# Kernel optimization log

Measured on AMD Instinct MI355X. Metric: run time of the kernel, lower is better.

The kernel has to match this reference:

```python
import math
import jax, jax.numpy as jnp
import numpy as np

NUM_BINS = 8
TRANS = 8
LEFT, RIGHT = -1.0, 1.0
MIN_W = MIN_H = MIN_D = 1.0e-4


def setup_inputs() -> dict:
    key = jax.random.key(0)
    ks = jax.random.split(key, 8)
    B, D, H, OUT = 524288, 16, 256, TRANS * (3 * NUM_BINS - 1)
    x = jax.random.uniform(ks[0], (B, D), jnp.float32, -0.99, 0.99)
    W0 = jax.random.normal(ks[1], (8, H), jnp.float32) * (1.0 / math.sqrt(8))
    b0 = jnp.zeros((H,), jnp.float32)
    W1 = jax.random.normal(ks[2], (H, H), jnp.float32) * (1.0 / math.sqrt(H))
    b1 = jnp.zeros((H,), jnp.float32)
    Wout = jax.random.normal(ks[3], (H, OUT), jnp.float32) * (0.1 / math.sqrt(H))
    bout = jnp.zeros((OUT,), jnp.float32)
    return {"x": x, "W0": W0, "b0": b0, "W1": W1, "b1": b1, "Wout": Wout, "bout": bout}


def _rq_spline(x, raw_w, raw_h, raw_d):
    # x: [B, T]; raw_w/raw_h: [B, T, K]; raw_d: [B, T, K-1]
    span = RIGHT - LEFT
    const = math.log(math.exp(1.0 - MIN_D) - 1.0)
    widths = jax.nn.softmax(raw_w, axis=-1)
    heights = jax.nn.softmax(raw_h, axis=-1)
    derivs = jax.nn.softplus(raw_d + const) + MIN_D
    widths = span * (MIN_W + (1.0 - MIN_W * NUM_BINS) * widths)
    heights = span * (MIN_H + (1.0 - MIN_H * NUM_BINS) * heights)
    edge_x = LEFT + jnp.pad(jnp.cumsum(widths, axis=-1), ((0, 0), (0, 0), (1, 0)))
    edge_y = LEFT + jnp.pad(jnp.cumsum(heights, axis=-1), ((0, 0), (0, 0), (1, 0)))
    derivs = jnp.pad(derivs, ((0, 0), (0, 0), (1, 1)), constant_values=1.0)
    out_mask = (x <= LEFT + 1e-3) | (x >= RIGHT - 1e-3)
    x_in = jnp.where(out_mask, 0.0, x)
    # searchsorted(right=True) - 1 == count of edges <= x_in, minus 1
    idx = jnp.clip(jnp.sum(edge_x <= x_in[..., None], axis=-1) - 1, 0, NUM_BINS - 1)
    g = lambda a: jnp.take_along_axis(a, idx[..., None], axis=-1)[..., 0]
    xk, yk = g(edge_x), g(edge_y)
    wk, hk = g(widths), g(heights)
    dk, dk1 = g(derivs), g(derivs[..., 1:])
    sk = hk / wk
    eps = (x_in - xk) / wk
    eps_term = eps * (1.0 - eps)
    eps2 = eps * eps
    beta = sk + (dk1 + dk - 2.0 * sk) * eps_term
    alpha = hk * (sk * eps2 + dk * eps_term)
    output = jnp.where(out_mask, x, yk + alpha / beta)
    logdet = (2.0 * jnp.log(sk)
              + jnp.log(dk1 * eps2 + 2.0 * sk * eps_term + dk * (1.0 - eps) ** 2)
              - 2.0 * jnp.log(beta))
    logdet = jnp.where(out_mask, 0.0, logdet)
    return output, logdet


def reference(x, W0, b0, W1, b1, Wout, bout):
    x1 = x[..., :TRANS]   # transformed half (mask == True)
    x2 = x[..., TRANS:]   # conditioning half
    h = jax.nn.relu(x2 @ W0 + b0)
    h = jax.nn.relu(h @ W1 + b1)
    raw = (h @ Wout + bout).reshape(x.shape[0], TRANS, 3 * NUM_BINS - 1)
    raw_w = raw[..., :NUM_BINS]
    raw_h = raw[..., NUM_BINS:2 * NUM_BINS]
    raw_d = raw[..., 2 * NUM_BINS:]
    y1, logdet = _rq_spline(x1, raw_w, raw_h, raw_d)
    out = jnp.concatenate([y1, x2], axis=-1)
    return out, jnp.sum(logdet, axis=-1)
```

## Files before the change

### kernel.cpp

```cpp
#include <hip/hip_runtime.h>
#include <hip/hip_bf16.h>


typedef __bf16 bf16x8 __attribute__((ext_vector_type(8)));
typedef float  f32x4  __attribute__((ext_vector_type(4)));

#define MFMA16(a,b,c) __builtin_amdgcn_mfma_f32_16x16x32_bf16((a),(b),(c),0,0,0)

#define SW_W1_OFF 8192
#define SW_WO_OFF 73728
#define SW_TOTAL  122880

#define HSTRIDE 264
#define RSTRIDE 200

__global__ void prep_kernel(const float* __restrict__ W0,
                            const float* __restrict__ W1,
                            const float* __restrict__ Wout,
                            __bf16* __restrict__ sw)
{
  int i = blockIdx.x * 256 + threadIdx.x;
  if (i >= SW_TOTAL) return;
  const float* src; int K, N, NT, li;
  if (i < SW_W1_OFF)      { src = W0;   K = 8;   N = 256; NT = 16; li = i; }
  else if (i < SW_WO_OFF) { src = W1;   K = 256; N = 256; NT = 16; li = i - SW_W1_OFF; }
  else                    { src = Wout; K = 256; N = 184; NT = 12; li = i - SW_WO_OFF; }
  int j    = li & 7;
  int l    = (li >> 3) & 63;
  int rest = li >> 9;
  int nt   = rest % NT;
  int kb   = rest / NT;
  int k = kb * 32 + ((l >> 4) << 3) + j;
  int n = nt * 16 + (l & 15);
  float v = (k < K && n < N) ? src[k * N + n] : 0.0f;
  sw[i] = (__bf16)v;
}

__global__ __launch_bounds__(512, 4)
void fused_kernel(const float* __restrict__ x,
                  const float* __restrict__ b0v,
                  const float* __restrict__ b1v,
                  const float* __restrict__ boutv,
                  const __bf16* __restrict__ sw,
                  float* __restrict__ out,
                  int nrows)
{
  __shared__ __align__(16) unsigned char smem[2 * 64 * HSTRIDE * 2];
  __bf16* h1   = (__bf16*)smem;
  __bf16* h2   = (__bf16*)(smem + 64 * HSTRIDE * 2);
  __bf16* rawb = h1;
  float*  ldet = (float*)h2;

  const int tid  = threadIdx.x;
  const int wave = tid >> 6;
  const int lane = tid & 63;
  const int quad = lane >> 4;
  const int l16  = lane & 15;
  const int row0 = blockIdx.x * 64;

  const __bf16* swW1 = sw + SW_W1_OFF;
  const __bf16* swWo = sw + SW_WO_OFF;

  const f32x4 z4 = {0.f, 0.f, 0.f, 0.f};

  {
    bf16x8 a1[4];
    #pragma unroll
    for (int mt = 0; mt < 4; mt++){
      const float* xp = x + (long)(row0 + mt*16 + l16) * 16 + 8;
      float4 u = *(const float4*)xp;
      float4 v = *(const float4*)(xp + 4);
      bf16x8 a;
      a[0]=(__bf16)u.x; a[1]=(__bf16)u.y; a[2]=(__bf16)u.z; a[3]=(__bf16)u.w;
      a[4]=(__bf16)v.x; a[5]=(__bf16)v.y; a[6]=(__bf16)v.z; a[7]=(__bf16)v.w;
      a1[mt] = a;
    }
    f32x4 acc[4][2];
    #pragma unroll
    for (int mt=0;mt<4;mt++){ acc[mt][0]=z4; acc[mt][1]=z4; }
    #pragma unroll
    for (int nt=0;nt<2;nt++){
      int ntg = wave*2 + nt;
      bf16x8 b = *(const bf16x8*)(sw + (ntg*64 + lane)*8);
      #pragma unroll
      for (int mt=0;mt<4;mt++) acc[mt][nt] = MFMA16(a1[mt], b, acc[mt][nt]);
    }
    #pragma unroll
    for (int nt=0;nt<2;nt++){
      int col = wave*32 + nt*16 + l16;
      float bias = b0v[col];
      #pragma unroll
      for (int mt=0;mt<4;mt++)
        #pragma unroll
        for (int r=0;r<4;r++){
          int row = mt*16 + quad*4 + r;
          h1[row*HSTRIDE + col] = (__bf16)fmaxf(acc[mt][nt][r] + bias, 0.f);
        }
    }
  }
  __syncthreads();

  {
    f32x4 acc[4][2];
    #pragma unroll
    for (int mt=0;mt<4;mt++){ acc[mt][0]=z4; acc[mt][1]=z4; }
    #pragma unroll
    for (int kb=0;kb<8;kb++){
      bf16x8 af[4];
      #pragma unroll
      for (int mt=0;mt<4;mt++){
        int row = mt*16 + l16;
        af[mt] = *(const bf16x8*)(h1 + row*HSTRIDE + kb*32 + quad*8);
      }
      #pragma unroll
      for (int nt=0;nt<2;nt++){
        int ntg = wave*2 + nt;
        bf16x8 b = *(const bf16x8*)(swW1 + ((kb*16 + ntg)*64 + lane)*8);
        #pragma unroll
        for (int mt=0;mt<4;mt++) acc[mt][nt] = MFMA16(af[mt], b, acc[mt][nt]);
      }
    }
    #pragma unroll
    for (int nt=0;nt<2;nt++){
      int col = wave*32 + nt*16 + l16;
      float bias = b1v[col];
      #pragma unroll
      for (int mt=0;mt<4;mt++)
        #pragma unroll
        for (int r=0;r<4;r++){
          int row = mt*16 + quad*4 + r;
          h2[row*HSTRIDE + col] = (__bf16)fmaxf(acc[mt][nt][r] + bias, 0.f);
        }
    }
  }
  __syncthreads();

  {
    f32x4 acc[4][2];
    #pragma unroll
    for (int mt=0;mt<4;mt++){ acc[mt][0]=z4; acc[mt][1]=z4; }
    const bool has2 = (wave < 4);
    #pragma unroll
    for (int kb=0;kb<8;kb++){
      bf16x8 af[4];
      #pragma unroll
      for (int mt=0;mt<4;mt++){
        int row = mt*16 + l16;
        af[mt] = *(const bf16x8*)(h2 + row*HSTRIDE + kb*32 + quad*8);
      }
      bf16x8 b0 = *(const bf16x8*)(swWo + ((kb*12 + wave)*64 + lane)*8);
      #pragma unroll
      for (int mt=0;mt<4;mt++) acc[mt][0] = MFMA16(af[mt], b0, acc[mt][0]);
      if (has2){
        bf16x8 b1 = *(const bf16x8*)(swWo + ((kb*12 + wave + 8)*64 + lane)*8);
        #pragma unroll
        for (int mt=0;mt<4;mt++) acc[mt][1] = MFMA16(af[mt], b1, acc[mt][1]);
      }
    }
    #pragma unroll
    for (int s=0;s<2;s++){
      if (s == 1 && !has2) break;
      int ntg = s ? (wave + 8) : wave;
      int col = ntg*16 + l16;
      if (col < 184){
        int t = (col * 713) >> 14;
        float bias = boutv[col];
        #pragma unroll
        for (int mt=0;mt<4;mt++)
          #pragma unroll
          for (int r=0;r<4;r++){
            int row = mt*16 + quad*4 + r;
            rawb[row*RSTRIDE + col + t] = (__bf16)(acc[mt][s][r] + bias);
          }
      }
    }
  }
  __syncthreads();

  {
    int row = tid >> 3;
    int t   = tid & 7;
    long gr = row0 + row;
    float xv = x[gr*16 + t];
    out[gr*16 + 8 + t] = x[gr*16 + 8 + t];

    const __bf16* rr = rawb + row*RSTRIDE + t*24;
    bf16x8 v0 = *(const bf16x8*)(rr);
    bf16x8 v1 = *(const bf16x8*)(rr + 8);
    bf16x8 v2 = *(const bf16x8*)(rr + 16);

    float ew[8], eh[8];
    float sw_ = 0.f, sh_ = 0.f;
    #pragma unroll
    for (int i=0;i<8;i++){ ew[i] = __expf((float)v0[i]); sw_ += ew[i]; }
    #pragma unroll
    for (int i=0;i<8;i++){ eh[i] = __expf((float)v1[i]); sh_ += eh[i]; }
    float cw = 1.9984f * __builtin_amdgcn_rcpf(sw_);
    float ch = 1.9984f * __builtin_amdgcn_rcpf(sh_);

    float d[9];
    d[0] = 1.f; d[8] = 1.f;
    #pragma unroll
    for (int i=0;i<7;i++){
      float z = (float)v2[i] + 0.54116666f;
      d[i+1] = fmaxf(z, 0.f) + __logf(1.f + __expf(-fabsf(z))) + 1e-4f;
    }

    bool msk = (xv <= -0.999f) || (xv >= 0.999f);
    float xin = msk ? 0.f : xv;

    float w_i = fmaf(ew[0], cw, 2e-4f);
    float h_i = fmaf(eh[0], ch, 2e-4f);
    float edge = -1.f + w_i, cy = -1.f + h_i;
    float xk = -1.f, yk = -1.f, wk = w_i, hk = h_i, dk = d[0], dk1 = d[1];
    #pragma unroll
    for (int i=1;i<8;i++){
      w_i = fmaf(ew[i], cw, 2e-4f);
      h_i = fmaf(eh[i], ch, 2e-4f);
      bool le = (edge <= xin);
      xk  = le ? edge : xk;
      yk  = le ? cy   : yk;
      wk  = le ? w_i  : wk;
      hk  = le ? h_i  : hk;
      dk  = le ? d[i] : dk;
      dk1 = le ? d[i+1] : dk1;
      edge += w_i; cy += h_i;
    }

    float rwk = __builtin_amdgcn_rcpf(wk);
    float sk  = hk * rwk;
    float eps = (xin - xk) * rwk;
    float om  = 1.f - eps;
    float et  = eps * om;
    float e2  = eps * eps;
    float beta  = sk + (dk1 + dk - 2.f*sk) * et;
    float rb    = __builtin_amdgcn_rcpf(beta);
    float alpha = hk * (sk*e2 + dk*et);
    float yv  = msk ? xv : (yk + alpha * rb);
    float num = dk1*e2 + 2.f*sk*et + dk*om*om;
    float arg = sk*sk*num*rb*rb;
    float ld  = msk ? 0.f : __logf(arg);

    out[gr*16 + t] = yv;
    ldet[tid] = ld;
  }
  __syncthreads();

  if (tid < 64){
    float s = 0.f;
    #pragma unroll
    for (int t=0;t<8;t++) s += ldet[tid*8 + t];
    out[(long)nrows*16 + row0 + tid] = s;
  }
}

extern "C" void kernel_launch(void* const* d_in, const int* in_sizes, int n_in,
                              void* d_out, int out_size, void* d_ws, size_t ws_size,
                              hipStream_t stream)
{
  const float* x    = (const float*)d_in[0];
  const float* W0   = (const float*)d_in[1];
  const float* b0   = (const float*)d_in[2];
  const float* W1   = (const float*)d_in[3];
  const float* b1   = (const float*)d_in[4];
  const float* Wout = (const float*)d_in[5];
  const float* bout = (const float*)d_in[6];
  float* out = (float*)d_out;
  __bf16* sw = (__bf16*)d_ws;

  int nrows = in_sizes[0] / 16;
  int ntiles = nrows / 64;

  prep_kernel<<<(SW_TOTAL + 255)/256, 256, 0, stream>>>(W0, W1, Wout, sw);
  fused_kernel<<<ntiles, 512, 0, stream>>>(x, b0, b1, bout, sw, out, nrows);
}
```

Measured before the change: 271.4 us.

## Transpose MLP layer GEMMs so weights are the A operand with vectorized activation stores

The first two layers are rewritten to compute the transposed product, with weights as the MFMA A operand and activations as B. Each lane's accumulator then holds four consecutive hidden features for one row, so bias loads become float4 and the activation stores to LDS become 8-byte vector writes instead of scalar bf16 writes. The output layer is retiled so each wave covers a 2x3 tile grid with no idle waves, and the raw buffer reuses the 264 stride. The cost is a zero-padded layer-0 operand where only quad 0 loads x, and more global weight fragment loads per wave in layer 1.

```diff
diff --git a/kernel.cpp b/kernel.cpp
--- a/kernel.cpp
+++ b/kernel.cpp
@@ -3,6 +3,7 @@
 
 
 typedef __bf16 bf16x8 __attribute__((ext_vector_type(8)));
+typedef __bf16 bf16x4 __attribute__((ext_vector_type(4)));
 typedef float  f32x4  __attribute__((ext_vector_type(4)));
 
 #define MFMA16(a,b,c) __builtin_amdgcn_mfma_f32_16x16x32_bf16((a),(b),(c),0,0,0)
@@ -12,7 +13,6 @@
 #define SW_TOTAL  122880
 
 #define HSTRIDE 264
-#define RSTRIDE 200
 
 __global__ void prep_kernel(const float* __restrict__ W0,
                             const float* __restrict__ W1,
@@ -60,117 +60,110 @@
 
   const __bf16* swW1 = sw + SW_W1_OFF;
   const __bf16* swWo = sw + SW_WO_OFF;
-
   const f32x4 z4 = {0.f, 0.f, 0.f, 0.f};
 
-  {
-    bf16x8 a1[4];
-    #pragma unroll
-    for (int mt = 0; mt < 4; mt++){
-      const float* xp = x + (long)(row0 + mt*16 + l16) * 16 + 8;
-      float4 u = *(const float4*)xp;
-      float4 v = *(const float4*)(xp + 4);
-      bf16x8 a;
-      a[0]=(__bf16)u.x; a[1]=(__bf16)u.y; a[2]=(__bf16)u.z; a[3]=(__bf16)u.w;
-      a[4]=(__bf16)v.x; a[5]=(__bf16)v.y; a[6]=(__bf16)v.z; a[7]=(__bf16)v.w;
-      a1[mt] = a;
-    }
+  const int mq = wave >> 1;
+  const int nh = wave & 1;
+
+  {
+    bf16x8 bfr[2];
+    #pragma unroll
+    for (int nt = 0; nt < 2; nt++){
+      bf16x8 b = {};
+      if (quad == 0){
+        const float* xp = x + (long)(row0 + (nh*2 + nt)*16 + l16)*16 + 8;
+        float4 u = *(const float4*)xp;
+        float4 v = *(const float4*)(xp + 4);
+        b[0]=(__bf16)u.x; b[1]=(__bf16)u.y; b[2]=(__bf16)u.z; b[3]=(__bf16)u.w;
+        b[4]=(__bf16)v.x; b[5]=(__bf16)v.y; b[6]=(__bf16)v.z; b[7]=(__bf16)v.w;
+      }
+      bfr[nt] = b;
+    }
+    #pragma unroll
+    for (int mi = 0; mi < 4; mi++){
+      int mt = mq*4 + mi;
+      bf16x8 a = *(const bf16x8*)(sw + (mt*64 + lane)*8);
+      f32x4 acc0 = MFMA16(a, bfr[0], z4);
+      f32x4 acc1 = MFMA16(a, bfr[1], z4);
+      float4 bb = *(const float4*)(b0v + mt*16 + quad*4);
+      bf16x4 p0, p1;
+      p0[0]=(__bf16)fmaxf(acc0[0]+bb.x,0.f); p0[1]=(__bf16)fmaxf(acc0[1]+bb.y,0.f);
+      p0[2]=(__bf16)fmaxf(acc0[2]+bb.z,0.f); p0[3]=(__bf16)fmaxf(acc0[3]+bb.w,0.f);
+      p1[0]=(__bf16)fmaxf(acc1[0]+bb.x,0.f); p1[1]=(__bf16)fmaxf(acc1[1]+bb.y,0.f);
+      p1[2]=(__bf16)fmaxf(acc1[2]+bb.z,0.f); p1[3]=(__bf16)fmaxf(acc1[3]+bb.w,0.f);
+      *(bf16x4*)(h1 + ((nh*2+0)*16 + l16)*HSTRIDE + mt*16 + quad*4) = p0;
+      *(bf16x4*)(h1 + ((nh*2+1)*16 + l16)*HSTRIDE + mt*16 + quad*4) = p1;
+    }
+  }
+  __syncthreads();
+
+  {
     f32x4 acc[4][2];
     #pragma unroll
-    for (int mt=0;mt<4;mt++){ acc[mt][0]=z4; acc[mt][1]=z4; }
-    #pragma unroll
-    for (int nt=0;nt<2;nt++){
-      int ntg = wave*2 + nt;
-      bf16x8 b = *(const bf16x8*)(sw + (ntg*64 + lane)*8);
-      #pragma unroll
-      for (int mt=0;mt<4;mt++) acc[mt][nt] = MFMA16(a1[mt], b, acc[mt][nt]);
-    }
-    #pragma unroll
-    for (int nt=0;nt<2;nt++){
-      int col = wave*32 + nt*16 + l16;
-      float bias = b0v[col];
-      #pragma unroll
-      for (int mt=0;mt<4;mt++)
-        #pragma unroll
-        for (int r=0;r<4;r++){
-          int row = mt*16 + quad*4 + r;
-          h1[row*HSTRIDE + col] = (__bf16)fmaxf(acc[mt][nt][r] + bias, 0.f);
-        }
-    }
-  }
-  __syncthreads();
-
-  {
-    f32x4 acc[4][2];
-    #pragma unroll
-    for (int mt=0;mt<4;mt++){ acc[mt][0]=z4; acc[mt][1]=z4; }
+    for (int mi=0;mi<4;mi++){ acc[mi][0]=z4; acc[mi][1]=z4; }
     #pragma unroll
     for (int kb=0;kb<8;kb++){
-      bf16x8 af[4];
-      #pragma unroll
-      for (int mt=0;mt<4;mt++){
-        int row = mt*16 + l16;
-        af[mt] = *(const bf16x8*)(h1 + row*HSTRIDE + kb*32 + quad*8);
-      }
+      bf16x8 bfr[2];
+      #pragma unroll
+      for (int nt=0;nt<2;nt++)
+        bfr[nt] = *(const bf16x8*)(h1 + ((nh*2+nt)*16 + l16)*HSTRIDE + kb*32 + quad*8);
+      #pragma unroll
+      for (int mi=0;mi<4;mi++){
+        bf16x8 a = *(const bf16x8*)(swW1 + ((kb*16 + mq*4 + mi)*64 + lane)*8);
+        acc[mi][0] = MFMA16(a, bfr[0], acc[mi][0]);
+        acc[mi][1] = MFMA16(a, bfr[1], acc[mi][1]);
+      }
+    }
+    #pragma unroll
+    for (int mi=0;mi<4;mi++){
+      int mt = mq*4 + mi;
+      float4 bb = *(const float4*)(b1v + mt*16 + quad*4);
       #pragma unroll
       for (int nt=0;nt<2;nt++){
-        int ntg = wave*2 + nt;
-        bf16x8 b = *(const bf16x8*)(swW1 + ((kb*16 + ntg)*64 + lane)*8);
-        #pragma unroll
-        for (int mt=0;mt<4;mt++) acc[mt][nt] = MFMA16(af[mt], b, acc[mt][nt]);
-      }
-    }
-    #pragma unroll
-    for (int nt=0;nt<2;nt++){
-      int col = wave*32 + nt*16 + l16;
-      float bias = b1v[col];
-      #pragma unroll
-      for (int mt=0;mt<4;mt++)
-        #pragma unroll
-        for (int r=0;r<4;r++){
-          int row = mt*16 + quad*4 + r;
-          h2[row*HSTRIDE + col] = (__bf16)fmaxf(acc[mt][nt][r] + bias, 0.f);
-        }
-    }
-  }
-  __syncthreads();
-
-  {
-    f32x4 acc[4][2];
-    #pragma unroll
-    for (int mt=0;mt<4;mt++){ acc[mt][0]=z4; acc[mt][1]=z4; }
-    const bool has2 = (wave < 4);
+        bf16x4 p;
+        p[0]=(__bf16)fmaxf(acc[mi][nt][0]+bb.x,0.f);
+        p[1]=(__bf16)fmaxf(acc[mi][nt][1]+bb.y,0.f);
+        p[2]=(__bf16)fmaxf(acc[mi][nt][2]+bb.z,0.f);
+        p[3]=(__bf16)fmaxf(acc[mi][nt][3]+bb.w,0.f);
+        *(bf16x4*)(h2 + ((nh*2+nt)*16 + l16)*HSTRIDE + mt*16 + quad*4) = p;
+      }
+    }
+  }
+  __syncthreads();
+
+  {
+    const int mh = wave >> 2;
+    const int nc = wave & 3;
+    f32x4 acc[2][3];
+    #pragma unroll
+    for (int mi=0;mi<2;mi++)
+      #pragma unroll
+      for (int ni=0;ni<3;ni++) acc[mi][ni] = z4;
     #pragma unroll
     for (int kb=0;kb<8;kb++){
-      bf16x8 af[4];
-      #pragma unroll
-      for (int mt=0;mt<4;mt++){
-        int row = mt*16 + l16;
-        af[mt] = *(const bf16x8*)(h2 + row*HSTRIDE + kb*32 + quad*8);
-      }
-      bf16x8 b0 = *(const bf16x8*)(swWo + ((kb*12 + wave)*64 + lane)*8);
-      #pragma unroll
-      for (int mt=0;mt<4;mt++) acc[mt][0] = MFMA16(af[mt], b0, acc[mt][0]);
-      if (has2){
-        bf16x8 b1 = *(const bf16x8*)(swWo + ((kb*12 + wave + 8)*64 + lane)*8);
-        #pragma unroll
-        for (int mt=0;mt<4;mt++) acc[mt][1] = MFMA16(af[mt], b1, acc[mt][1]);
-      }
-    }
-    #pragma unroll
-    for (int s=0;s<2;s++){
-      if (s == 1 && !has2) break;
-      int ntg = s ? (wave + 8) : wave;
-      int col = ntg*16 + l16;
+      bf16x8 af[2];
+      #pragma unroll
+      for (int mi=0;mi<2;mi++)
+        af[mi] = *(const bf16x8*)(h2 + ((mh*2+mi)*16 + l16)*HSTRIDE + kb*32 + quad*8);
+      #pragma unroll
+      for (int ni=0;ni<3;ni++){
+        bf16x8 b = *(const bf16x8*)(swWo + ((kb*12 + nc*3 + ni)*64 + lane)*8);
+        acc[0][ni] = MFMA16(af[0], b, acc[0][ni]);
+        acc[1][ni] = MFMA16(af[1], b, acc[1][ni]);
+      }
+    }
+    #pragma unroll
+    for (int ni=0;ni<3;ni++){
+      int col = (nc*3 + ni)*16 + l16;
       if (col < 184){
         int t = (col * 713) >> 14;
         float bias = boutv[col];
         #pragma unroll
-        for (int mt=0;mt<4;mt++)
+        for (int mi=0;mi<2;mi++)
           #pragma unroll
           for (int r=0;r<4;r++){
-            int row = mt*16 + quad*4 + r;
-            rawb[row*RSTRIDE + col + t] = (__bf16)(acc[mt][s][r] + bias);
+            int row = (mh*2+mi)*16 + quad*4 + r;
+            rawb[row*HSTRIDE + col + t] = (__bf16)(acc[mi][ni][r] + bias);
           }
       }
     }
@@ -184,7 +177,7 @@
     float xv = x[gr*16 + t];
     out[gr*16 + 8 + t] = x[gr*16 + 8 + t];
 
-    const __bf16* rr = rawb + row*RSTRIDE + t*24;
+    const __bf16* rr = rawb + row*HSTRIDE + t*24;
     bf16x8 v0 = *(const bf16x8*)(rr);
     bf16x8 v1 = *(const bf16x8*)(rr + 8);
     bf16x8 v2 = *(const bf16x8*)(rr + 16);
```

After: 265.6 us. 2.1% less time.
